# Optimization experiments

Hardware: AMD Instinct MI355X
Metric: run time of the kernel (lower is better)

## Reference

```python
import jax, jax.numpy as jnp
import numpy as np

NEG_SLOPE_ATT = 0.2   # PyG GATConv attention LeakyReLU slope
NEG_SLOPE_ACT = 0.01  # F.leaky_relu default slope (applied after encoder)


def gat_conv(x, edge_index, W, a_src, a_dst, b, concat=True):
    """PyG-style GATConv with add_self_loops=True.
    x: [N, Fin], edge_index: [2, E] (row 0 = source j, row 1 = target i).
    W: [Fin, H*C], a_src/a_dst: [H, C], b: [H*C] (concat) or [C].
    """
    N = x.shape[0]
    H, C = a_src.shape
    h = (x @ W).reshape(N, H, C)                      # [N, H, C]
    alpha_s = jnp.einsum('nhc,hc->nh', h, a_src)      # [N, H]
    alpha_d = jnp.einsum('nhc,hc->nh', h, a_dst)      # [N, H]
    loop = jnp.arange(N, dtype=edge_index.dtype)
    src = jnp.concatenate([edge_index[0], loop])       # self loops appended
    dst = jnp.concatenate([edge_index[1], loop])
    e = jax.nn.leaky_relu(alpha_s[src] + alpha_d[dst], NEG_SLOPE_ATT)  # [E', H]
    # segment softmax over edges sharing the same target node
    m = jax.ops.segment_max(e, dst, num_segments=N)    # [N, H]
    ex = jnp.exp(e - m[dst])
    denom = jax.ops.segment_sum(ex, dst, num_segments=N)  # [N, H]
    att = ex / denom[dst]                              # [E', H]
    out = jax.ops.segment_sum(att[:, :, None] * h[src], dst, num_segments=N)  # [N, H, C]
    out = out.reshape(N, H * C) if concat else out.mean(axis=1)
    return out + b


def setup_inputs() -> dict:
    key = jax.random.key(0)
    ks = jax.random.split(key, 16)
    N, E = 50000, 800000
    in_dim, hidden, heads, out_dim, n_layers = 16, 16, 8, 3, 3
    hd = heads * hidden  # 128
    s = 0.1
    inp = {
        'x': jax.random.normal(ks[0], (N, in_dim), jnp.float32),
        'edge_index': jax.random.randint(ks[1], (2, E), 0, N, jnp.int64),
        'enc_W': jax.random.normal(ks[2], (in_dim, hd), jnp.float32) * s,
        'enc_as': jax.random.normal(ks[3], (heads, hidden), jnp.float32) * s,
        'enc_ad': jax.random.normal(ks[4], (heads, hidden), jnp.float32) * s,
        'enc_b': jnp.zeros((hd,), jnp.float32),
        'hid_W': jax.random.normal(ks[5], (n_layers, hd, hd), jnp.float32) * s,
        'hid_as': jax.random.normal(ks[6], (n_layers, heads, hidden), jnp.float32) * s,
        'hid_ad': jax.random.normal(ks[7], (n_layers, heads, hidden), jnp.float32) * s,
        'hid_b': jnp.zeros((n_layers, hd), jnp.float32),
        'dec_W': jax.random.normal(ks[8], (hd, out_dim), jnp.float32) * s,
        'dec_as': jax.random.normal(ks[9], (1, out_dim), jnp.float32) * s,
        'dec_ad': jax.random.normal(ks[10], (1, out_dim), jnp.float32) * s,
        'dec_b': jnp.zeros((out_dim,), jnp.float32),
    }
    return inp


def reference(x, edge_index, enc_W, enc_as, enc_ad, enc_b,
              hid_W, hid_as, hid_ad, hid_b, dec_W, dec_as, dec_ad, dec_b):
    h = gat_conv(x, edge_index, enc_W, enc_as, enc_ad, enc_b)
    h = jax.nn.leaky_relu(h, NEG_SLOPE_ACT)
    for i in range(hid_W.shape[0]):
        h = gat_conv(h, edge_index, hid_W[i], hid_as[i], hid_ad[i], hid_b[i])
    out = gat_conv(h, edge_index, dec_W, dec_as, dec_ad, dec_b)  # heads=1, concat
    return out
```

## Files before the change

### kernel.cpp

```cpp
#include <hip/hip_runtime.h>
#include <hip/hip_fp16.h>
#include <float.h>
#include <math.h>

#define NEG_ATT 0.2f
#define NEG_ACT 0.01f
#define BK 512
#define NBMAX 128

__device__ __forceinline__ float lrelu(float v, float s) { return v >= 0.f ? v : s * v; }

struct __align__(16) H8 { __half2 a, b, c, d; };
struct __align__(8)  H4 { __half2 x, y; };

typedef _Float16 f16;
typedef f16 f16x8 __attribute__((ext_vector_type(8)));
typedef float f32x4 __attribute__((ext_vector_type(4)));

__global__ __launch_bounds__(256) void k_front(
    const float* __restrict__ x, const float* __restrict__ W,
    const float* __restrict__ a_src, const float* __restrict__ a_dst,
    __half* __restrict__ gh, float* __restrict__ as_out, float* __restrict__ ad_out,
    const float* __restrict__ hid_W, const float* __restrict__ hid_as,
    const float* __restrict__ hid_ad, __half* __restrict__ Wt,
    const int* __restrict__ ei, int* __restrict__ hist_part,
    int N, int E, int L, int nbEnc, int nbPrep) {
  __shared__ float sh[16 * 128 + 64 * 20];
  int tid = threadIdx.x;
  int bid = blockIdx.x;

  if (bid >= nbEnc + nbPrep) {
    int* lc = (int*)sh;
    if (tid < NBMAX) lc[tid] = 0;
    __syncthreads();
    int base = (bid - nbEnc - nbPrep) * 1024;
    #pragma unroll
    for (int j = 0; j < 4; ++j) {
      int e = base + j * 256 + tid;
      if (e < E) atomicAdd(&lc[ei[E + e] >> 9], 1);
    }
    __syncthreads();
    if (tid < NBMAX) hist_part[(size_t)(bid - nbEnc - nbPrep) * NBMAX + tid] = lc[tid];
    return;
  }
  if (bid >= nbEnc) {
    int idx = (bid - nbEnc) * 256 + tid;
    if (idx < L * 144 * 128) {
      int l = idx / (144 * 128);
      int rem = idx - l * 144 * 128;
      int r = rem >> 7, kk = rem & 127;
      const float* Wl = hid_W + (size_t)l * 128 * 128;
      float v;
      if (r < 128) {
        v = Wl[kk * 128 + r];
      } else {
        int hd = r - 128;
        const float* a = (hd < 8) ? (hid_as + (size_t)l * 128) : (hid_ad + (size_t)l * 128);
        int h2 = hd & 7;
        v = 0.f;
        #pragma unroll
        for (int c = 0; c < 16; ++c) v += Wl[kk * 128 + h2 * 16 + c] * a[h2 * 16 + c];
      }
      Wt[(size_t)l * 144 * 128 + r * 128 + kk] = __float2half(v);
    }
    return;
  }

  const int K = 16, KP = 20;
  float* Wl = sh;
  float* xl = sh + 16 * 128;
  int n0 = bid * 64;
  for (int i = tid * 4; i < (K << 6); i += 1024) {
    int row = i >> 4;
    int c = i & 15;
    float4 v = make_float4(0.f, 0.f, 0.f, 0.f);
    if (n0 + row < N) v = *(const float4*)(x + (size_t)(n0 + row) * K + c);
    *(float4*)(xl + row * KP + c) = v;
  }
  for (int i = tid * 4; i < 2048; i += 1024)
    *(float4*)(Wl + i) = *(const float4*)(W + i);
  __syncthreads();

  int ng = tid >> 4, jg = tid & 15;
  int jlo = jg * 4, jhi = 64 + jg * 4;
  float alo[4][4] = {}, ahi[4][4] = {};
  #pragma unroll 4
  for (int kk = 0; kk < K; ++kk) {
    const float4 wlo = *(const float4*)(Wl + (kk << 7) + jlo);
    const float4 whi = *(const float4*)(Wl + (kk << 7) + jhi);
    const float* xr = xl + (ng * 4) * KP + kk;
    #pragma unroll
    for (int i = 0; i < 4; ++i) {
      float xv = xr[i * KP];
      alo[i][0] += xv * wlo.x; alo[i][1] += xv * wlo.y;
      alo[i][2] += xv * wlo.z; alo[i][3] += xv * wlo.w;
      ahi[i][0] += xv * whi.x; ahi[i][1] += xv * whi.y;
      ahi[i][2] += xv * whi.z; ahi[i][3] += xv * whi.w;
    }
  }

  int hlo = jg >> 2, hhi = 4 + (jg >> 2), off4 = (jg & 3) * 4;
  #pragma unroll
  for (int i = 0; i < 4; ++i) {
    int n = n0 + ng * 4 + i;
    if (n >= N) break;
    H4 plo = { __floats2half2_rn(alo[i][0], alo[i][1]), __floats2half2_rn(alo[i][2], alo[i][3]) };
    H4 phi = { __floats2half2_rn(ahi[i][0], ahi[i][1]), __floats2half2_rn(ahi[i][2], ahi[i][3]) };
    *(H4*)(gh + (size_t)n * 128 + jlo) = plo;
    *(H4*)(gh + (size_t)n * 128 + jhi) = phi;
    float ps_lo = 0.f, pd_lo = 0.f, ps_hi = 0.f, pd_hi = 0.f;
    #pragma unroll
    for (int t = 0; t < 4; ++t) {
      ps_lo += alo[i][t] * a_src[hlo * 16 + off4 + t];
      pd_lo += alo[i][t] * a_dst[hlo * 16 + off4 + t];
      ps_hi += ahi[i][t] * a_src[hhi * 16 + off4 + t];
      pd_hi += ahi[i][t] * a_dst[hhi * 16 + off4 + t];
    }
    ps_lo += __shfl_xor(ps_lo, 1); ps_lo += __shfl_xor(ps_lo, 2);
    pd_lo += __shfl_xor(pd_lo, 1); pd_lo += __shfl_xor(pd_lo, 2);
    ps_hi += __shfl_xor(ps_hi, 1); ps_hi += __shfl_xor(ps_hi, 2);
    pd_hi += __shfl_xor(pd_hi, 1); pd_hi += __shfl_xor(pd_hi, 2);
    if ((jg & 3) == 0) {
      as_out[n * 8 + hlo] = ps_lo; ad_out[n * 8 + hlo] = pd_lo;
      as_out[n * 8 + hhi] = ps_hi; ad_out[n * 8 + hhi] = pd_hi;
    }
  }
}

__global__ __launch_bounds__(1024) void k_bscan2(
    const int* __restrict__ hist_part, int nbHist,
    int* pair_st, int* bucket_st, int* pair_cur, int N, int NB) {
  __shared__ int part[1024];
  __shared__ int t1[128], t2[128];
  int tid = threadIdx.x;
  int colp = tid & 127, rg = tid >> 7;
  int s = 0;
  for (int r = rg; r < nbHist; r += 8) s += hist_part[(size_t)r * NBMAX + colp];
  part[tid] = s;
  __syncthreads();
  int c = 0, nodesb = 0;
  if (tid < 128) {
    #pragma unroll
    for (int j = 0; j < 8; ++j) c += part[j * 128 + tid];
    if (tid < NB) {
      int base = tid * BK;
      nodesb = (N - base < BK) ? (N - base) : BK;
    }
    t1[tid] = c;
    t2[tid] = c + nodesb;
  }
  __syncthreads();
  for (int off = 1; off < 128; off <<= 1) {
    int a = 0, b = 0;
    if (tid < 128 && tid >= off) { a = t1[tid - off]; b = t2[tid - off]; }
    __syncthreads();
    if (tid < 128) { t1[tid] += a; t2[tid] += b; }
    __syncthreads();
  }
  if (tid < NB) {
    int ps = t1[tid] - c, bs = t2[tid] - (c + nodesb);
    pair_st[tid] = ps; pair_cur[tid] = ps; bucket_st[tid] = bs;
  }
  if (tid == 127) { pair_st[NB] = t1[127]; bucket_st[NB] = t2[127]; }
}

__global__ __launch_bounds__(1024) void k_bappend(const int* __restrict__ ei,
                                                  int* __restrict__ pair_cur,
                                                  int* __restrict__ pairs, int E, int NB) {
  __shared__ int lc[NBMAX], lb[NBMAX];
  int tid = threadIdx.x;
  if (tid < NB) lc[tid] = 0;
  __syncthreads();
  int e = blockIdx.x * 1024 + tid;
  int b = 0, r = 0, s = 0, d = 0;
  bool valid = e < E;
  if (valid) {
    s = ei[e]; d = ei[E + e]; b = d >> 9;
    r = atomicAdd(&lc[b], 1);
  }
  __syncthreads();
  if (tid < NB && lc[tid]) lb[tid] = atomicAdd(&pair_cur[tid], lc[tid]);
  __syncthreads();
  if (valid) pairs[lb[b] + r] = s | ((d & (BK - 1)) << 17);
}

__global__ __launch_bounds__(1024) void k_bbuild(const int* __restrict__ pairs,
    const int* __restrict__ pair_start, const int* __restrict__ bucket_start,
    int* __restrict__ row_ptr, int* __restrict__ colb, int N, int NB) {
  __shared__ int deg[BK], tmp[1024], cur[BK];
  int b = blockIdx.x, tid = threadIdx.x;
  int base = b * BK;
  int nodesb = (N - base < BK) ? (N - base) : BK;
  if (tid < BK) deg[tid] = (tid < nodesb) ? 1 : 0;
  __syncthreads();
  int p0 = pair_start[b], p1 = pair_start[b + 1];
  for (int p = p0 + tid; p < p1; p += 1024)
    atomicAdd(&deg[pairs[p] >> 17], 1);
  __syncthreads();
  int v = (tid < BK) ? deg[tid] : 0;
  tmp[tid] = v;
  __syncthreads();
  for (int off = 1; off < 1024; off <<= 1) {
    int t = (tid >= off) ? tmp[tid - off] : 0;
    __syncthreads();
    tmp[tid] += t;
    __syncthreads();
  }
  int bs = bucket_start[b];
  if (tid < nodesb) {
    int ex = tmp[tid] - v;
    row_ptr[base + tid] = bs + ex;
    colb[bs + ex] = base + tid;
    cur[tid] = ex + 1;
  }
  if (b == 0 && tid == 0) row_ptr[N] = bucket_start[NB];
  __syncthreads();
  for (int p = p0 + tid; p < p1; p += 1024) {
    int pr = pairs[p];
    int r = atomicAdd(&cur[pr >> 17], 1);
    colb[bs + r] = pr & 0x1FFFF;
  }
}

__global__ __launch_bounds__(256) void k_gemm_hid_mfma(
    const __half* __restrict__ xh_g, const __half* __restrict__ Wt_g,
    __half* __restrict__ gh, float* __restrict__ as_out, float* __restrict__ ad_out,
    int N) {
  __shared__ __half xh[64][136];
  __shared__ __half wt[144][136];
  int tid = threadIdx.x;
  int n0 = blockIdx.x * 64;

  for (int i = tid; i < 1024; i += 256) {
    int row = i >> 4, c8 = (i & 15) * 8;
    float4 v = make_float4(0.f, 0.f, 0.f, 0.f);
    if (n0 + row < N) v = *(const float4*)(xh_g + (size_t)(n0 + row) * 128 + c8);
    *(float4*)(&xh[row][c8]) = v;
  }
  for (int i = tid; i < 2304; i += 256) {
    int row = i >> 4, c8 = (i & 15) * 8;
    float4 v = *(const float4*)(Wt_g + (size_t)row * 128 + c8);
    *(float4*)(&wt[row][c8]) = v;
  }
  __syncthreads();

  int wave = tid >> 6, lane = tid & 63;
  int m = lane & 15, quad = lane >> 4;
  f32x4 acc[9] = {};
  #pragma unroll
  for (int kb = 0; kb < 128; kb += 32) {
    f16x8 a = *(const f16x8*)(&xh[wave * 16 + m][kb + quad * 8]);
    #pragma unroll
    for (int t = 0; t < 9; ++t) {
      f16x8 b = *(const f16x8*)(&wt[t * 16 + m][kb + quad * 8]);
      acc[t] = __builtin_amdgcn_mfma_f32_16x16x32_f16(a, b, acc[t], 0, 0, 0);
    }
  }

  #pragma unroll
  for (int r = 0; r < 4; ++r) {
    int node = n0 + wave * 16 + quad * 4 + r;
    if (node >= N) continue;
    #pragma unroll
    for (int t = 0; t < 8; ++t)
      gh[(size_t)node * 128 + t * 16 + m] = __float2half(acc[t][r]);
    float v = acc[8][r];
    if (m < 8) as_out[node * 8 + m] = v;
    else       ad_out[node * 8 + (m - 8)] = v;
  }
}

__global__ __launch_bounds__(256) void k_agg128(
    const int* __restrict__ row_ptr, const int* __restrict__ col,
    const float* __restrict__ as, const float* __restrict__ ad,
    const __half* __restrict__ gh, const float* __restrict__ bias,
    __half* __restrict__ out, int N, int act,
    int dec, const float* __restrict__ dWd, const float* __restrict__ dasd,
    const float* __restrict__ dadd, float4* __restrict__ g4, float* __restrict__ adn) {
  int wid = threadIdx.x >> 6;
  int lane = threadIdx.x & 63;
  int n = blockIdx.x * 4 + wid;
  bool active = n < N;
  int nc = active ? n : 0;
  int s0 = active ? row_ptr[nc] : 0;
  int s1 = active ? row_ptr[nc + 1] : 0;

  int q = lane >> 4, l16 = lane & 15;
  int c0 = l16 * 8, hq = l16 >> 1;
  float adq = ad[nc * 8 + hq];
  const __half* gq = gh + c0;
  const float* asq = as + hq;
  float den = 0.f;
  float t0 = 0.f, t1 = 0.f, t2 = 0.f, t3 = 0.f, t4 = 0.f, t5 = 0.f, t6 = 0.f, t7 = 0.f;

  int b = s0;
  for (; b + 16 <= s1; b += 16) {
    int e0 = b + q, e1 = b + 4 + q, e2 = b + 8 + q, e3 = b + 12 + q;
    int sa = col[e0], sb = col[e1], sc = col[e2], sd = col[e3];
    float aa = asq[sa * 8], ab = asq[sb * 8], ac = asq[sc * 8], ae = asq[sd * 8];
    H8 ha = *(const H8*)(gq + (size_t)sa * 128);
    H8 hb = *(const H8*)(gq + (size_t)sb * 128);
    H8 hc = *(const H8*)(gq + (size_t)sc * 128);
    H8 hd = *(const H8*)(gq + (size_t)sd * 128);
    float wa = __expf(lrelu(aa + adq, NEG_ATT));
    float wb = __expf(lrelu(ab + adq, NEG_ATT));
    float wc = __expf(lrelu(ac + adq, NEG_ATT));
    float wd = __expf(lrelu(ae + adq, NEG_ATT));
    den += wa + wb + wc + wd;
    float2 f;
    f = __half22float2(ha.a); t0 += wa * f.x; t1 += wa * f.y;
    f = __half22float2(ha.b); t2 += wa * f.x; t3 += wa * f.y;
    f = __half22float2(ha.c); t4 += wa * f.x; t5 += wa * f.y;
    f = __half22float2(ha.d); t6 += wa * f.x; t7 += wa * f.y;
    f = __half22float2(hb.a); t0 += wb * f.x; t1 += wb * f.y;
    f = __half22float2(hb.b); t2 += wb * f.x; t3 += wb * f.y;
    f = __half22float2(hb.c); t4 += wb * f.x; t5 += wb * f.y;
    f = __half22float2(hb.d); t6 += wb * f.x; t7 += wb * f.y;
    f = __half22float2(hc.a); t0 += wc * f.x; t1 += wc * f.y;
    f = __half22float2(hc.b); t2 += wc * f.x; t3 += wc * f.y;
    f = __half22float2(hc.c); t4 += wc * f.x; t5 += wc * f.y;
    f = __half22float2(hc.d); t6 += wc * f.x; t7 += wc * f.y;
    f = __half22float2(hd.a); t0 += wd * f.x; t1 += wd * f.y;
    f = __half22float2(hd.b); t2 += wd * f.x; t3 += wd * f.y;
    f = __half22float2(hd.c); t4 += wd * f.x; t5 += wd * f.y;
    f = __half22float2(hd.d); t6 += wd * f.x; t7 += wd * f.y;
  }
  for (; b + 4 <= s1; b += 4) {
    int e0 = b + q;
    int sa = col[e0];
    float aa = asq[sa * 8];
    H8 ha = *(const H8*)(gq + (size_t)sa * 128);
    float wa = __expf(lrelu(aa + adq, NEG_ATT));
    den += wa;
    float2 f;
    f = __half22float2(ha.a); t0 += wa * f.x; t1 += wa * f.y;
    f = __half22float2(ha.b); t2 += wa * f.x; t3 += wa * f.y;
    f = __half22float2(ha.c); t4 += wa * f.x; t5 += wa * f.y;
    f = __half22float2(ha.d); t6 += wa * f.x; t7 += wa * f.y;
  }
  if (b + q < s1) {
    int e0 = b + q;
    int sa = col[e0];
    float aa = asq[sa * 8];
    H8 ha = *(const H8*)(gq + (size_t)sa * 128);
    float wa = __expf(lrelu(aa + adq, NEG_ATT));
    den += wa;
    float2 f;
    f = __half22float2(ha.a); t0 += wa * f.x; t1 += wa * f.y;
    f = __half22float2(ha.b); t2 += wa * f.x; t3 += wa * f.y;
    f = __half22float2(ha.c); t4 += wa * f.x; t5 += wa * f.y;
    f = __half22float2(ha.d); t6 += wa * f.x; t7 += wa * f.y;
  }

  den += __shfl_xor(den, 16); den += __shfl_xor(den, 32);
  t0 += __shfl_xor(t0, 16); t0 += __shfl_xor(t0, 32);
  t1 += __shfl_xor(t1, 16); t1 += __shfl_xor(t1, 32);
  t2 += __shfl_xor(t2, 16); t2 += __shfl_xor(t2, 32);
  t3 += __shfl_xor(t3, 16); t3 += __shfl_xor(t3, 32);
  t4 += __shfl_xor(t4, 16); t4 += __shfl_xor(t4, 32);
  t5 += __shfl_xor(t5, 16); t5 += __shfl_xor(t5, 32);
  t6 += __shfl_xor(t6, 16); t6 += __shfl_xor(t6, 32);
  t7 += __shfl_xor(t7, 16); t7 += __shfl_xor(t7, 32);

  float inv = 1.f / den;
  const float4 b0 = *(const float4*)(bias + c0);
  const float4 b1 = *(const float4*)(bias + c0 + 4);
  float o0 = t0 * inv + b0.x, o1 = t1 * inv + b0.y;
  float o2 = t2 * inv + b0.z, o3 = t3 * inv + b0.w;
  float o4 = t4 * inv + b1.x, o5 = t5 * inv + b1.y;
  float o6 = t6 * inv + b1.z, o7 = t7 * inv + b1.w;
  if (act) {
    o0 = lrelu(o0, NEG_ACT); o1 = lrelu(o1, NEG_ACT);
    o2 = lrelu(o2, NEG_ACT); o3 = lrelu(o3, NEG_ACT);
    o4 = lrelu(o4, NEG_ACT); o5 = lrelu(o5, NEG_ACT);
    o6 = lrelu(o6, NEG_ACT); o7 = lrelu(o7, NEG_ACT);
  }
  if (!dec) {
    if (active && q == 0) {
      H8 pk = { __floats2half2_rn(o0, o1), __floats2half2_rn(o2, o3),
                __floats2half2_rn(o4, o5), __floats2half2_rn(o6, o7) };
      *(H8*)(out + (size_t)n * 128 + c0) = pk;
    }
  } else {
    float ov[8] = {o0, o1, o2, o3, o4, o5, o6, o7};
    float p0 = 0.f, p1 = 0.f, p2 = 0.f;
    #pragma unroll
    for (int i = 0; i < 8; ++i) {
      float wv0 = dWd[(c0 + i) * 3], wv1 = dWd[(c0 + i) * 3 + 1], wv2 = dWd[(c0 + i) * 3 + 2];
      p0 += ov[i] * wv0; p1 += ov[i] * wv1; p2 += ov[i] * wv2;
    }
    p0 += __shfl_xor(p0, 1); p0 += __shfl_xor(p0, 2); p0 += __shfl_xor(p0, 4); p0 += __shfl_xor(p0, 8);
    p1 += __shfl_xor(p1, 1); p1 += __shfl_xor(p1, 2); p1 += __shfl_xor(p1, 4); p1 += __shfl_xor(p1, 8);
    p2 += __shfl_xor(p2, 1); p2 += __shfl_xor(p2, 2); p2 += __shfl_xor(p2, 4); p2 += __shfl_xor(p2, 8);
    if (active && lane == 0) {
      float as_n = p0 * dasd[0] + p1 * dasd[1] + p2 * dasd[2];
      float ad_n = p0 * dadd[0] + p1 * dadd[1] + p2 * dadd[2];
      g4[n] = make_float4(p0, p1, p2, as_n);
      adn[n] = ad_n;
    }
  }
}

__global__ __launch_bounds__(256) void k_dec_agg(
    const int* __restrict__ row_ptr, const int* __restrict__ col,
    const float* __restrict__ ad, const float4* __restrict__ g4,
    const float* __restrict__ b, float* __restrict__ out, int N) {
  int n = blockIdx.x * blockDim.x + threadIdx.x;
  if (n >= N) return;
  int s0 = row_ptr[n], s1 = row_ptr[n + 1];
  float adv = ad[n];
  float den = 0.f, A0 = 0.f, A1 = 0.f, A2 = 0.f;
  int k = s0;
  for (; k + 4 <= s1; k += 4) {
    int sa = col[k], sb = col[k + 1], sc = col[k + 2], sd = col[k + 3];
    float4 v0 = g4[sa], v1 = g4[sb], v2 = g4[sc], v3 = g4[sd];
    float w0 = __expf(lrelu(v0.w + adv, NEG_ATT));
    float w1 = __expf(lrelu(v1.w + adv, NEG_ATT));
    float w2 = __expf(lrelu(v2.w + adv, NEG_ATT));
    float w3 = __expf(lrelu(v3.w + adv, NEG_ATT));
    den += w0 + w1 + w2 + w3;
    A0 += w0 * v0.x + w1 * v1.x + w2 * v2.x + w3 * v3.x;
    A1 += w0 * v0.y + w1 * v1.y + w2 * v2.y + w3 * v3.y;
    A2 += w0 * v0.z + w1 * v1.z + w2 * v2.z + w3 * v3.z;
  }
  for (; k < s1; ++k) {
    float4 v = g4[col[k]];
    float w = __expf(lrelu(v.w + adv, NEG_ATT));
    den += w;
    A0 += w * v.x; A1 += w * v.y; A2 += w * v.z;
  }
  float inv = 1.f / den;
  out[(size_t)n * 3]     = A0 * inv + b[0];
  out[(size_t)n * 3 + 1] = A1 * inv + b[1];
  out[(size_t)n * 3 + 2] = A2 * inv + b[2];
}

extern "C" void kernel_launch(void* const* d_in, const int* in_sizes, int n_in,
                              void* d_out, int out_size, void* d_ws, size_t ws_size,
                              hipStream_t stream) {
  const float* x      = (const float*)d_in[0];
  const int*   ei     = (const int*)d_in[1];
  const float* enc_W  = (const float*)d_in[2];
  const float* enc_as = (const float*)d_in[3];
  const float* enc_ad = (const float*)d_in[4];
  const float* enc_b  = (const float*)d_in[5];
  const float* hid_W  = (const float*)d_in[6];
  const float* hid_as = (const float*)d_in[7];
  const float* hid_ad = (const float*)d_in[8];
  const float* hid_b  = (const float*)d_in[9];
  const float* dec_W  = (const float*)d_in[10];
  const float* dec_as = (const float*)d_in[11];
  const float* dec_ad = (const float*)d_in[12];
  const float* dec_b  = (const float*)d_in[13];

  const int N = in_sizes[0] / 16;
  const int E = in_sizes[1] / 2;
  const int L = in_sizes[6] / (128 * 128);
  const int NB = (N + BK - 1) / BK;

  char* wbase = (char*)d_ws;
  size_t woff = 0;
  auto walloc = [&](size_t bytes, size_t align) -> void* {
    woff = (woff + align - 1) & ~(align - 1);
    void* p = wbase + woff;
    woff += bytes;
    return p;
  };
  const int nbEnc  = (N + 63) / 64;
  const int nbPrep = (L * 144 * 128 + 255) / 256;
  const int nbHist = (E + 1023) / 1024;

  __half* gh        = (__half*)walloc((size_t)N * 128 * 2, 16);
  __half* hh        = (__half*)walloc((size_t)N * 128 * 2, 16);
  float*  as_buf    = (float*)walloc((size_t)N * 8 * 4, 16);
  float*  ad_buf    = (float*)walloc((size_t)N * 8 * 4, 16);
  float4* g4        = (float4*)walloc((size_t)N * 16, 16);
  float*  adn       = (float*)walloc((size_t)N * 4, 16);
  __half* Wt_g      = (__half*)walloc((size_t)3 * 144 * 128 * 2, 16);
  int*    row_ptr   = (int*)walloc((size_t)(N + 1) * 4, 4);
  int*    colb      = (int*)walloc((size_t)(E + N) * 4, 4);
  int*    pairs     = (int*)walloc((size_t)E * 4, 4);
  int*    hist_part = (int*)walloc((size_t)nbHist * NBMAX * 4, 4);
  int*    pair_st   = (int*)walloc((NBMAX + 1) * 4, 4);
  int*    bucket_st = (int*)walloc((NBMAX + 1) * 4, 4);
  int*    pair_cur  = (int*)walloc((NBMAX + 1) * 4, 4);

  const dim3 b256(256);
  const dim3 gFront(nbEnc + nbPrep + nbHist);
  const dim3 gGemm(nbEnc);
  const dim3 gAgg((N + 3) / 4);
  const dim3 gNode((N + 255) / 256);

  k_front<<<gFront, b256, 0, stream>>>(x, enc_W, enc_as, enc_ad, gh, as_buf, ad_buf,
                                       hid_W, hid_as, hid_ad, Wt_g, ei, hist_part,
                                       N, E, L, nbEnc, nbPrep);
  k_bscan2<<<dim3(1), dim3(1024), 0, stream>>>(hist_part, nbHist, pair_st, bucket_st,
                                               pair_cur, N, NB);
  k_bappend<<<dim3(nbHist), dim3(1024), 0, stream>>>(ei, pair_cur, pairs, E, NB);
  k_bbuild<<<dim3(NB), dim3(1024), 0, stream>>>(pairs, pair_st, bucket_st, row_ptr, colb, N, NB);

  k_agg128<<<gAgg, b256, 0, stream>>>(row_ptr, colb, as_buf, ad_buf, gh, enc_b, hh, N, 1,
                                      0, nullptr, nullptr, nullptr, nullptr, nullptr);

  for (int l = 0; l < L; ++l) {
    k_gemm_hid_mfma<<<gGemm, b256, 0, stream>>>(hh, Wt_g + (size_t)l * 144 * 128,
                                                gh, as_buf, ad_buf, N);
    int dec = (l == L - 1) ? 1 : 0;
    k_agg128<<<gAgg, b256, 0, stream>>>(row_ptr, colb, as_buf, ad_buf, gh,
                                        hid_b + (size_t)l * 128, hh, N, 0,
                                        dec, dec_W, dec_as, dec_ad, g4, adn);
  }

  k_dec_agg<<<gNode, b256, 0, stream>>>(row_ptr, colb, adn, g4, dec_b,
                                        (float*)d_out, N);
}
```

Before: 357.5 us.

## Store node features head-major and aggregate one head per block

Node features and attention scores move from node-major to head-major slices ([H][N][16]). The aggregation kernel now handles one head per block, with blockIdx low bits selecting the head, so each head's 50000×16 half slice (about 1.6 MB) is gathered on its own and may stay in cache. The decoder projection, previously fused into the last aggregation, becomes a separate k_dec_gemm kernel. The cost is 8x more aggregation blocks, with the row_ptr/col indices and attention weights read once per head instead of once per node, plus an extra launch.

```diff
diff --git a/kernel.cpp b/kernel.cpp
--- a/kernel.cpp
+++ b/kernel.cpp
@@ -20,7 +20,7 @@
 __global__ __launch_bounds__(256) void k_front(
     const float* __restrict__ x, const float* __restrict__ W,
     const float* __restrict__ a_src, const float* __restrict__ a_dst,
-    __half* __restrict__ gh, float* __restrict__ as_out, float* __restrict__ ad_out,
+    __half* __restrict__ ghs, float* __restrict__ as_h, float* __restrict__ ad_h,
     const float* __restrict__ hid_W, const float* __restrict__ hid_as,
     const float* __restrict__ hid_ad, __half* __restrict__ Wt,
     const int* __restrict__ ei, int* __restrict__ hist_part,
@@ -106,8 +106,8 @@
     if (n >= N) break;
     H4 plo = { __floats2half2_rn(alo[i][0], alo[i][1]), __floats2half2_rn(alo[i][2], alo[i][3]) };
     H4 phi = { __floats2half2_rn(ahi[i][0], ahi[i][1]), __floats2half2_rn(ahi[i][2], ahi[i][3]) };
-    *(H4*)(gh + (size_t)n * 128 + jlo) = plo;
-    *(H4*)(gh + (size_t)n * 128 + jhi) = phi;
+    *(H4*)(ghs + ((size_t)hlo * N + n) * 16 + off4) = plo;
+    *(H4*)(ghs + ((size_t)hhi * N + n) * 16 + off4) = phi;
     float ps_lo = 0.f, pd_lo = 0.f, ps_hi = 0.f, pd_hi = 0.f;
     #pragma unroll
     for (int t = 0; t < 4; ++t) {
@@ -121,8 +121,8 @@
     ps_hi += __shfl_xor(ps_hi, 1); ps_hi += __shfl_xor(ps_hi, 2);
     pd_hi += __shfl_xor(pd_hi, 1); pd_hi += __shfl_xor(pd_hi, 2);
     if ((jg & 3) == 0) {
-      as_out[n * 8 + hlo] = ps_lo; ad_out[n * 8 + hlo] = pd_lo;
-      as_out[n * 8 + hhi] = ps_hi; ad_out[n * 8 + hhi] = pd_hi;
+      as_h[(size_t)hlo * N + n] = ps_lo; ad_h[(size_t)hlo * N + n] = pd_lo;
+      as_h[(size_t)hhi * N + n] = ps_hi; ad_h[(size_t)hhi * N + n] = pd_hi;
     }
   }
 }
@@ -223,8 +223,8 @@
 }
 
 __global__ __launch_bounds__(256) void k_gemm_hid_mfma(
-    const __half* __restrict__ xh_g, const __half* __restrict__ Wt_g,
-    __half* __restrict__ gh, float* __restrict__ as_out, float* __restrict__ ad_out,
+    const __half* __restrict__ hhs, const __half* __restrict__ Wt_g,
+    __half* __restrict__ ghs, float* __restrict__ as_h, float* __restrict__ ad_h,
     int N) {
   __shared__ __half xh[64][136];
   __shared__ __half wt[144][136];
@@ -232,10 +232,12 @@
   int n0 = blockIdx.x * 64;
 
   for (int i = tid; i < 1024; i += 256) {
-    int row = i >> 4, c8 = (i & 15) * 8;
+    int hs = i >> 7, chunk = i & 127;
+    int row = chunk >> 1, hf = chunk & 1;
     float4 v = make_float4(0.f, 0.f, 0.f, 0.f);
-    if (n0 + row < N) v = *(const float4*)(xh_g + (size_t)(n0 + row) * 128 + c8);
-    *(float4*)(&xh[row][c8]) = v;
+    int node = n0 + row;
+    if (node < N) v = *(const float4*)(hhs + ((size_t)hs * N + node) * 16 + hf * 8);
+    *(float4*)(&xh[row][hs * 16 + hf * 8]) = v;
   }
   for (int i = tid; i < 2304; i += 256) {
     int row = i >> 4, c8 = (i & 15) * 8;
@@ -263,142 +265,101 @@
     if (node >= N) continue;
     #pragma unroll
     for (int t = 0; t < 8; ++t)
-      gh[(size_t)node * 128 + t * 16 + m] = __float2half(acc[t][r]);
+      ghs[((size_t)t * N + node) * 16 + m] = __float2half(acc[t][r]);
     float v = acc[8][r];
-    if (m < 8) as_out[node * 8 + m] = v;
-    else       ad_out[node * 8 + (m - 8)] = v;
-  }
-}
-
-__global__ __launch_bounds__(256) void k_agg128(
+    if (m < 8) as_h[(size_t)m * N + node] = v;
+    else       ad_h[(size_t)(m - 8) * N + node] = v;
+  }
+}
+
+__global__ __launch_bounds__(256) void k_agg_slice(
     const int* __restrict__ row_ptr, const int* __restrict__ col,
-    const float* __restrict__ as, const float* __restrict__ ad,
-    const __half* __restrict__ gh, const float* __restrict__ bias,
-    __half* __restrict__ out, int N, int act,
-    int dec, const float* __restrict__ dWd, const float* __restrict__ dasd,
-    const float* __restrict__ dadd, float4* __restrict__ g4, float* __restrict__ adn) {
-  int wid = threadIdx.x >> 6;
-  int lane = threadIdx.x & 63;
-  int n = blockIdx.x * 4 + wid;
+    const float* __restrict__ as_h, const float* __restrict__ ad_h,
+    const __half* __restrict__ ghs, const float* __restrict__ bias,
+    __half* __restrict__ hhs, int N, int act) {
+  int h = blockIdx.x & 7;
+  int nb = blockIdx.x >> 3;
+  int wv = threadIdx.x >> 6, lane = threadIdx.x & 63;
+  int n = nb * 4 + wv;
   bool active = n < N;
   int nc = active ? n : 0;
-  int s0 = active ? row_ptr[nc] : 0;
-  int s1 = active ? row_ptr[nc + 1] : 0;
-
-  int q = lane >> 4, l16 = lane & 15;
-  int c0 = l16 * 8, hq = l16 >> 1;
-  float adq = ad[nc * 8 + hq];
-  const __half* gq = gh + c0;
-  const float* asq = as + hq;
-  float den = 0.f;
-  float t0 = 0.f, t1 = 0.f, t2 = 0.f, t3 = 0.f, t4 = 0.f, t5 = 0.f, t6 = 0.f, t7 = 0.f;
-
-  int b = s0;
-  for (; b + 16 <= s1; b += 16) {
-    int e0 = b + q, e1 = b + 4 + q, e2 = b + 8 + q, e3 = b + 12 + q;
-    int sa = col[e0], sb = col[e1], sc = col[e2], sd = col[e3];
-    float aa = asq[sa * 8], ab = asq[sb * 8], ac = asq[sc * 8], ae = asq[sd * 8];
-    H8 ha = *(const H8*)(gq + (size_t)sa * 128);
-    H8 hb = *(const H8*)(gq + (size_t)sb * 128);
-    H8 hc = *(const H8*)(gq + (size_t)sc * 128);
-    H8 hd = *(const H8*)(gq + (size_t)sd * 128);
-    float wa = __expf(lrelu(aa + adq, NEG_ATT));
-    float wb = __expf(lrelu(ab + adq, NEG_ATT));
-    float wc = __expf(lrelu(ac + adq, NEG_ATT));
-    float wd = __expf(lrelu(ae + adq, NEG_ATT));
-    den += wa + wb + wc + wd;
-    float2 f;
-    f = __half22float2(ha.a); t0 += wa * f.x; t1 += wa * f.y;
-    f = __half22float2(ha.b); t2 += wa * f.x; t3 += wa * f.y;
-    f = __half22float2(ha.c); t4 += wa * f.x; t5 += wa * f.y;
-    f = __half22float2(ha.d); t6 += wa * f.x; t7 += wa * f.y;
-    f = __half22float2(hb.a); t0 += wb * f.x; t1 += wb * f.y;
-    f = __half22float2(hb.b); t2 += wb * f.x; t3 += wb * f.y;
-    f = __half22float2(hb.c); t4 += wb * f.x; t5 += wb * f.y;
-    f = __half22float2(hb.d); t6 += wb * f.x; t7 += wb * f.y;
-    f = __half22float2(hc.a); t0 += wc * f.x; t1 += wc * f.y;
-    f = __half22float2(hc.b); t2 += wc * f.x; t3 += wc * f.y;
-    f = __half22float2(hc.c); t4 += wc * f.x; t5 += wc * f.y;
-    f = __half22float2(hc.d); t6 += wc * f.x; t7 += wc * f.y;
-    f = __half22float2(hd.a); t0 += wd * f.x; t1 += wd * f.y;
-    f = __half22float2(hd.b); t2 += wd * f.x; t3 += wd * f.y;
-    f = __half22float2(hd.c); t4 += wd * f.x; t5 += wd * f.y;
-    f = __half22float2(hd.d); t6 += wd * f.x; t7 += wd * f.y;
-  }
-  for (; b + 4 <= s1; b += 4) {
-    int e0 = b + q;
-    int sa = col[e0];
-    float aa = asq[sa * 8];
-    H8 ha = *(const H8*)(gq + (size_t)sa * 128);
-    float wa = __expf(lrelu(aa + adq, NEG_ATT));
-    den += wa;
-    float2 f;
-    f = __half22float2(ha.a); t0 += wa * f.x; t1 += wa * f.y;
-    f = __half22float2(ha.b); t2 += wa * f.x; t3 += wa * f.y;
-    f = __half22float2(ha.c); t4 += wa * f.x; t5 += wa * f.y;
-    f = __half22float2(ha.d); t6 += wa * f.x; t7 += wa * f.y;
-  }
-  if (b + q < s1) {
-    int e0 = b + q;
-    int sa = col[e0];
-    float aa = asq[sa * 8];
-    H8 ha = *(const H8*)(gq + (size_t)sa * 128);
-    float wa = __expf(lrelu(aa + adq, NEG_ATT));
-    den += wa;
-    float2 f;
-    f = __half22float2(ha.a); t0 += wa * f.x; t1 += wa * f.y;
-    f = __half22float2(ha.b); t2 += wa * f.x; t3 += wa * f.y;
-    f = __half22float2(ha.c); t4 += wa * f.x; t5 += wa * f.y;
-    f = __half22float2(ha.d); t6 += wa * f.x; t7 += wa * f.y;
-  }
-
+  int s0 = row_ptr[nc];
+  int s1 = active ? row_ptr[nc + 1] : s0;
+
+  int eg = lane >> 2, cl = lane & 3;
+  const float* ash = as_h + (size_t)h * N;
+  float adv = ad_h[(size_t)h * N + nc];
+  const __half* gb = ghs + (size_t)h * N * 16 + cl * 4;
+
+  float den = 0.f, t0 = 0.f, t1 = 0.f, t2 = 0.f, t3 = 0.f;
+  for (int b = s0; b < s1; b += 16) {
+    int e = b + eg;
+    if (e < s1) {
+      int s = __builtin_nontemporal_load(col + e);
+      float aa = ash[s];
+      H4 hv = *(const H4*)(gb + (size_t)s * 16);
+      float w = __expf(lrelu(aa + adv, NEG_ATT));
+      den += w;
+      float2 f0 = __half22float2(hv.x), f1 = __half22float2(hv.y);
+      t0 += w * f0.x; t1 += w * f0.y; t2 += w * f1.x; t3 += w * f1.y;
+    }
+  }
+  den += __shfl_xor(den, 4); den += __shfl_xor(den, 8);
   den += __shfl_xor(den, 16); den += __shfl_xor(den, 32);
-  t0 += __shfl_xor(t0, 16); t0 += __shfl_xor(t0, 32);
-  t1 += __shfl_xor(t1, 16); t1 += __shfl_xor(t1, 32);
-  t2 += __shfl_xor(t2, 16); t2 += __shfl_xor(t2, 32);
-  t3 += __shfl_xor(t3, 16); t3 += __shfl_xor(t3, 32);
-  t4 += __shfl_xor(t4, 16); t4 += __shfl_xor(t4, 32);
-  t5 += __shfl_xor(t5, 16); t5 += __shfl_xor(t5, 32);
-  t6 += __shfl_xor(t6, 16); t6 += __shfl_xor(t6, 32);
-  t7 += __shfl_xor(t7, 16); t7 += __shfl_xor(t7, 32);
-
-  float inv = 1.f / den;
-  const float4 b0 = *(const float4*)(bias + c0);
-  const float4 b1 = *(const float4*)(bias + c0 + 4);
-  float o0 = t0 * inv + b0.x, o1 = t1 * inv + b0.y;
-  float o2 = t2 * inv + b0.z, o3 = t3 * inv + b0.w;
-  float o4 = t4 * inv + b1.x, o5 = t5 * inv + b1.y;
-  float o6 = t6 * inv + b1.z, o7 = t7 * inv + b1.w;
-  if (act) {
-    o0 = lrelu(o0, NEG_ACT); o1 = lrelu(o1, NEG_ACT);
-    o2 = lrelu(o2, NEG_ACT); o3 = lrelu(o3, NEG_ACT);
-    o4 = lrelu(o4, NEG_ACT); o5 = lrelu(o5, NEG_ACT);
-    o6 = lrelu(o6, NEG_ACT); o7 = lrelu(o7, NEG_ACT);
-  }
-  if (!dec) {
-    if (active && q == 0) {
-      H8 pk = { __floats2half2_rn(o0, o1), __floats2half2_rn(o2, o3),
-                __floats2half2_rn(o4, o5), __floats2half2_rn(o6, o7) };
-      *(H8*)(out + (size_t)n * 128 + c0) = pk;
-    }
-  } else {
-    float ov[8] = {o0, o1, o2, o3, o4, o5, o6, o7};
-    float p0 = 0.f, p1 = 0.f, p2 = 0.f;
-    #pragma unroll
-    for (int i = 0; i < 8; ++i) {
-      float wv0 = dWd[(c0 + i) * 3], wv1 = dWd[(c0 + i) * 3 + 1], wv2 = dWd[(c0 + i) * 3 + 2];
-      p0 += ov[i] * wv0; p1 += ov[i] * wv1; p2 += ov[i] * wv2;
-    }
-    p0 += __shfl_xor(p0, 1); p0 += __shfl_xor(p0, 2); p0 += __shfl_xor(p0, 4); p0 += __shfl_xor(p0, 8);
-    p1 += __shfl_xor(p1, 1); p1 += __shfl_xor(p1, 2); p1 += __shfl_xor(p1, 4); p1 += __shfl_xor(p1, 8);
-    p2 += __shfl_xor(p2, 1); p2 += __shfl_xor(p2, 2); p2 += __shfl_xor(p2, 4); p2 += __shfl_xor(p2, 8);
-    if (active && lane == 0) {
-      float as_n = p0 * dasd[0] + p1 * dasd[1] + p2 * dasd[2];
-      float ad_n = p0 * dadd[0] + p1 * dadd[1] + p2 * dadd[2];
-      g4[n] = make_float4(p0, p1, p2, as_n);
-      adn[n] = ad_n;
-    }
-  }
+  t0 += __shfl_xor(t0, 4); t0 += __shfl_xor(t0, 8); t0 += __shfl_xor(t0, 16); t0 += __shfl_xor(t0, 32);
+  t1 += __shfl_xor(t1, 4); t1 += __shfl_xor(t1, 8); t1 += __shfl_xor(t1, 16); t1 += __shfl_xor(t1, 32);
+  t2 += __shfl_xor(t2, 4); t2 += __shfl_xor(t2, 8); t2 += __shfl_xor(t2, 16); t2 += __shfl_xor(t2, 32);
+  t3 += __shfl_xor(t3, 4); t3 += __shfl_xor(t3, 8); t3 += __shfl_xor(t3, 16); t3 += __shfl_xor(t3, 32);
+
+  if (active && eg == 0) {
+    float inv = 1.f / den;
+    int c0 = h * 16 + cl * 4;
+    const float4 bv = *(const float4*)(bias + c0);
+    float o0 = t0 * inv + bv.x, o1 = t1 * inv + bv.y;
+    float o2 = t2 * inv + bv.z, o3 = t3 * inv + bv.w;
+    if (act) {
+      o0 = lrelu(o0, NEG_ACT); o1 = lrelu(o1, NEG_ACT);
+      o2 = lrelu(o2, NEG_ACT); o3 = lrelu(o3, NEG_ACT);
+    }
+    H4 pk = { __floats2half2_rn(o0, o1), __floats2half2_rn(o2, o3) };
+    *(H4*)(hhs + ((size_t)h * N + n) * 16 + cl * 4) = pk;
+  }
+}
+
+__global__ __launch_bounds__(256) void k_dec_gemm(
+    const __half* __restrict__ hhs, const float* __restrict__ Wd,
+    const float* __restrict__ asd, const float* __restrict__ add,
+    float4* __restrict__ g4, float* __restrict__ adn, int N) {
+  __shared__ float Wl[384];
+  int tid = threadIdx.x;
+  for (int i = tid; i < 384; i += 256) Wl[i] = Wd[i];
+  __syncthreads();
+  int n = blockIdx.x * 256 + tid;
+  if (n >= N) return;
+  float a0 = 0.f, a1 = 0.f, a2 = 0.f;
+  #pragma unroll
+  for (int h = 0; h < 8; ++h) {
+    #pragma unroll
+    for (int hf = 0; hf < 2; ++hf) {
+      H8 hv = *(const H8*)(hhs + ((size_t)h * N + n) * 16 + hf * 8);
+      int kbase = h * 16 + hf * 8;
+      float f[8];
+      float2 p;
+      p = __half22float2(hv.a); f[0] = p.x; f[1] = p.y;
+      p = __half22float2(hv.b); f[2] = p.x; f[3] = p.y;
+      p = __half22float2(hv.c); f[4] = p.x; f[5] = p.y;
+      p = __half22float2(hv.d); f[6] = p.x; f[7] = p.y;
+      #pragma unroll
+      for (int i = 0; i < 8; ++i) {
+        a0 += f[i] * Wl[(kbase + i) * 3];
+        a1 += f[i] * Wl[(kbase + i) * 3 + 1];
+        a2 += f[i] * Wl[(kbase + i) * 3 + 2];
+      }
+    }
+  }
+  float as_n = a0 * asd[0] + a1 * asd[1] + a2 * asd[2];
+  g4[n] = make_float4(a0, a1, a2, as_n);
+  adn[n] = a0 * add[0] + a1 * add[1] + a2 * add[2];
 }
 
 __global__ __launch_bounds__(256) void k_dec_agg(
@@ -470,10 +431,10 @@
   const int nbPrep = (L * 144 * 128 + 255) / 256;
   const int nbHist = (E + 1023) / 1024;
 
-  __half* gh        = (__half*)walloc((size_t)N * 128 * 2, 16);
-  __half* hh        = (__half*)walloc((size_t)N * 128 * 2, 16);
-  float*  as_buf    = (float*)walloc((size_t)N * 8 * 4, 16);
-  float*  ad_buf    = (float*)walloc((size_t)N * 8 * 4, 16);
+  __half* ghs       = (__half*)walloc((size_t)N * 128 * 2, 16);
+  __half* hhs       = (__half*)walloc((size_t)N * 128 * 2, 16);
+  float*  as_h      = (float*)walloc((size_t)N * 8 * 4, 16);
+  float*  ad_h      = (float*)walloc((size_t)N * 8 * 4, 16);
   float4* g4        = (float4*)walloc((size_t)N * 16, 16);
   float*  adn       = (float*)walloc((size_t)N * 4, 16);
   __half* Wt_g      = (__half*)walloc((size_t)3 * 144 * 128 * 2, 16);
@@ -488,10 +449,10 @@
   const dim3 b256(256);
   const dim3 gFront(nbEnc + nbPrep + nbHist);
   const dim3 gGemm(nbEnc);
-  const dim3 gAgg((N + 3) / 4);
+  const dim3 gAgg(((N + 3) / 4) * 8);
   const dim3 gNode((N + 255) / 256);
 
-  k_front<<<gFront, b256, 0, stream>>>(x, enc_W, enc_as, enc_ad, gh, as_buf, ad_buf,
+  k_front<<<gFront, b256, 0, stream>>>(x, enc_W, enc_as, enc_ad, ghs, as_h, ad_h,
                                        hid_W, hid_as, hid_ad, Wt_g, ei, hist_part,
                                        N, E, L, nbEnc, nbPrep);
   k_bscan2<<<dim3(1), dim3(1024), 0, stream>>>(hist_part, nbHist, pair_st, bucket_st,
@@ -499,18 +460,16 @@
   k_bappend<<<dim3(nbHist), dim3(1024), 0, stream>>>(ei, pair_cur, pairs, E, NB);
   k_bbuild<<<dim3(NB), dim3(1024), 0, stream>>>(pairs, pair_st, bucket_st, row_ptr, colb, N, NB);
 
-  k_agg128<<<gAgg, b256, 0, stream>>>(row_ptr, colb, as_buf, ad_buf, gh, enc_b, hh, N, 1,
-                                      0, nullptr, nullptr, nullptr, nullptr, nullptr);
+  k_agg_slice<<<gAgg, b256, 0, stream>>>(row_ptr, colb, as_h, ad_h, ghs, enc_b, hhs, N, 1);
 
   for (int l = 0; l < L; ++l) {
-    k_gemm_hid_mfma<<<gGemm, b256, 0, stream>>>(hh, Wt_g + (size_t)l * 144 * 128,
-                                                gh, as_buf, ad_buf, N);
-    int dec = (l == L - 1) ? 1 : 0;
-    k_agg128<<<gAgg, b256, 0, stream>>>(row_ptr, colb, as_buf, ad_buf, gh,
-                                        hid_b + (size_t)l * 128, hh, N, 0,
-                                        dec, dec_W, dec_as, dec_ad, g4, adn);
-  }
-
+    k_gemm_hid_mfma<<<gGemm, b256, 0, stream>>>(hhs, Wt_g + (size_t)l * 144 * 128,
+                                                ghs, as_h, ad_h, N);
+    k_agg_slice<<<gAgg, b256, 0, stream>>>(row_ptr, colb, as_h, ad_h, ghs,
+                                           hid_b + (size_t)l * 128, hhs, N, 0);
+  }
+
+  k_dec_gemm<<<gNode, b256, 0, stream>>>(hhs, dec_W, dec_as, dec_ad, g4, adn, N);
   k_dec_agg<<<gNode, b256, 0, stream>>>(row_ptr, colb, adn, g4, dec_b,
                                         (float*)d_out, N);
 }
```

After: 782.6 us. 119% more time.
